# Kernel tuning notes

Hardware: AMD Instinct MI355X
Metric: run time of the kernel (lower is better)

## Reference

```python
import jax, jax.numpy as jnp
import numpy as np

R = 5            # num_relations
NEG_SLOPE = 0.2
N1 = 30000       # layer0 target count
N2 = 15000       # layer1 target count


def brgcn_conv(x_src, x_tgt, edge_index, edge_type, Wj, Wi, att_j, att_i,
               Wq, Wk, Wv, sw, sb, Wrel, heads, outc):
    """One BRGCNConv layer: per-relation GAT edge softmax + bilevel relation attention."""
    N = x_tgt.shape[0]
    hc = heads * outc
    hj = (x_src @ Wj).reshape(-1, heads, outc)   # [Ns,H,C]
    hi = (x_tgt @ Wi).reshape(-1, heads, outc)   # [N,H,C]
    src, tgt = edge_index[0], edge_index[1]
    xj = hj[src]                                  # [E,H,C]
    xi = hi[tgt]                                  # [E,H,C]
    # relation-specific attention logits per edge
    aj = jnp.sum(att_j[edge_type] * xj, axis=-1)  # [E,H]
    ai = jnp.sum(att_i[edge_type] * xi, axis=-1)  # [E,H]
    alpha = jax.nn.leaky_relu(aj + ai, NEG_SLOPE)
    # edge softmax grouped by (target node, relation) == per-relation propagate
    seg = tgt * R + edge_type                     # [E]
    nseg = N * R
    amax = jax.ops.segment_max(alpha, seg, num_segments=nseg)
    amax = jnp.where(jnp.isfinite(amax), amax, 0.0)
    ex = jnp.exp(alpha - amax[seg])
    den = jax.ops.segment_sum(ex, seg, num_segments=nseg)
    w = ex / jnp.maximum(den[seg], 1e-16)         # [E,H]
    msg = (w[:, :, None] * xj).reshape(-1, hc)    # [E,H*C]
    z = jax.ops.segment_sum(msg, seg, num_segments=nseg)
    z = z.reshape(N, R, hc).transpose(1, 0, 2)    # [R,N,H*C]; zero rows where no edges
    # per-relation Q/K/V
    q = jnp.einsum('rnd,rde->rne', z, Wq).reshape(R, N, heads, outc)
    k = jnp.einsum('rnd,rde->rne', z, Wk).reshape(R, N, heads, outc)
    v = jnp.einsum('rnd,rde->rne', z, Wv).reshape(R, N, heads, outc)
    # bilevel relation attention: psi[r,s,n,h] = <q_r, k_s>
    psi = jnp.einsum('rnhc,snhc->rsnh', q, k)
    mask = (psi == 0) & (jnp.sum(psi, axis=1, keepdims=True) != 0)
    prob = jax.nn.softmax(jnp.where(mask, -jnp.inf, psi), axis=1)
    delta = jnp.einsum('rsnh,snhc->rnhc', prob, v).reshape(R, N, hc)
    out = jnp.einsum('rnd,r->nd', delta, Wrel[:, 0])
    # single node type -> node_self[0] applied to every target node
    return out + x_tgt @ sw + sb


def setup_inputs() -> dict:
    key = jax.random.key(0)
    ks = jax.random.split(key, 32)
    H0, C0, H1, C1 = 4, 64, 1, 40
    IN, HC0 = 128, H0 * C0
    NG, N0 = 200000, 100000
    E0, E1 = 300000, 150000
    f = lambda k, s: jax.random.normal(k, s, dtype=jnp.float32) * 0.05
    return dict(
        n_id=jax.random.randint(ks[1], (N0,), 0, NG),
        local_node_idx=jax.random.randint(ks[2], (NG,), 0, NG),
        node_type=jnp.zeros((NG,), dtype=jnp.int32),
        edge_index0=jax.random.randint(ks[3], (2, E0), 0, N1),
        edge_type0=jax.random.randint(ks[4], (E0,), 0, R),
        edge_index1=jax.random.randint(ks[5], (2, E1), 0, N2),
        edge_type1=jax.random.randint(ks[6], (E1,), 0, R),
        emb=f(ks[0], (NG, IN)),
        Wj0=f(ks[7], (IN, HC0)), Wi0=f(ks[8], (IN, HC0)),
        att_j0=f(ks[9], (R, H0, C0)), att_i0=f(ks[10], (R, H0, C0)),
        Wq0=f(ks[11], (R, HC0, HC0)), Wk0=f(ks[12], (R, HC0, HC0)), Wv0=f(ks[13], (R, HC0, HC0)),
        sw0=f(ks[14], (IN, HC0)), sb0=f(ks[15], (HC0,)), Wrel0=f(ks[16], (R, 1)),
        Wj1=f(ks[17], (HC0, C1)), Wi1=f(ks[18], (HC0, C1)),
        att_j1=f(ks[19], (R, H1, C1)), att_i1=f(ks[20], (R, H1, C1)),
        Wq1=f(ks[21], (R, C1, C1)), Wk1=f(ks[22], (R, C1, C1)), Wv1=f(ks[23], (R, C1, C1)),
        sw1=f(ks[24], (HC0, C1)), sb1=f(ks[25], (C1,)), Wrel1=f(ks[26], (R, 1)),
    )


def reference(n_id, local_node_idx, node_type, edge_index0, edge_type0,
              edge_index1, edge_type1, emb,
              Wj0, Wi0, att_j0, att_i0, Wq0, Wk0, Wv0, sw0, sb0, Wrel0,
              Wj1, Wi1, att_j1, att_i1, Wq1, Wk1, Wv1, sw1, sb1, Wrel1):
    # group_input: single node type, all features from the embedding table
    x = emb[local_node_idx[n_id]]
    x1 = brgcn_conv(x, x[:N1], edge_index0, edge_type0, Wj0, Wi0, att_j0, att_i0,
                    Wq0, Wk0, Wv0, sw0, sb0, Wrel0, heads=4, outc=64)
    x1 = jax.nn.relu(x1)  # dropout p=0 in eval
    x2 = brgcn_conv(x1, x1[:N2], edge_index1, edge_type1, Wj1, Wi1, att_j1, att_i1,
                    Wq1, Wk1, Wv1, sw1, sb1, Wrel1, heads=1, outc=40)
    return jax.nn.log_softmax(x2, axis=-1)
```

## Files before the change

### kernel.cpp

```cpp
#include <hip/hip_runtime.h>
#include <hip/hip_bf16.h>

#define DI __device__ __forceinline__

DI float b2f(unsigned short u) {
    union { unsigned int i; float f; } x; x.i = ((unsigned int)u) << 16; return x.f;
}
DI unsigned short f2b(float f) {
    union { float f; unsigned int i; } x; x.f = f;
    unsigned int r = x.i + 0x7fff + ((x.i >> 16) & 1);
    return (unsigned short)(r >> 16);
}
DI float ldin(const void* p, long i, int f32) {
    return f32 ? ((const float*)p)[i] : b2f(((const unsigned short*)p)[i]);
}
DI void stval(float* p, float v) { *p = v; }
DI void stval(unsigned short* p, float v) { *p = f2b(v); }

static constexpr int N1 = 30000, N2 = 15000, R = 5;
static constexpr int IN = 128, HC0 = 256, C1 = 40;
static constexpr float NEGBIG = -1e30f;
static constexpr int LDK = 64;

typedef short bf16x8 __attribute__((ext_vector_type(8)));
typedef float f32x4 __attribute__((ext_vector_type(4)));

__global__ void detect_k(const void* emb, int* flag)
{
    int lane = threadIdx.x;
    int bad = 0;
    for (int j = 0; j < 4; ++j) {
        float f = b2f(((const unsigned short*)emb)[lane * 4 + j]);
        if (!(fabsf(f) < 1e8f)) bad = 1;
    }
    unsigned long long anybad = __ballot(bad != 0);
    if (lane == 0) *flag = (anybad != 0ull) ? 1 : 0;
}

struct PrepJobs {
    const void* src[12];
    unsigned short* dst[12];
    int K[12];
    int N[12];
    int per[12];
};
__global__ __launch_bounds__(256) void prep_all_k(
    PrepJobs J,
    const void* aj0, const void* ai0, const void* aj1, const void* ai1,
    unsigned short* A0j, unsigned short* A0i, unsigned short* A1j, unsigned short* A1i,
    int* __restrict__ cnt, int cntn,
    const int* __restrict__ dflag)
{
    const int f32 = *dflag;
    const int y = blockIdx.y;
    long t = (long)blockIdx.x * 256 + threadIdx.x;
    if (y < 12) {
        if (t >= J.per[y]) return;
        const int K = J.K[y], N = J.N[y];
        long kn = (long)K * N;
        long b = t / kn, rem = t % kn;
        long k = rem / N, n = rem % N;
        J.dst[y][(b * N + n) * K + k] = f2b(ldin(J.src[y], t, f32));
    } else {
        if (t < 20 * 256) {
            int j = (int)(t >> 8), k = (int)(t & 255);
            int h = j & 3, r = j >> 2;
            bool on = (k >> 6) == h;
            A0j[t] = f2b(on ? ldin(aj0, r * 256 + k, f32) : 0.f);
            A0i[t] = f2b(on ? ldin(ai0, r * 256 + k, f32) : 0.f);
        }
        if (t < 5 * 40) {
            A1j[t] = f2b(ldin(aj1, t, f32));
            A1i[t] = f2b(ldin(ai1, t, f32));
        }
        if (t < cntn) cnt[t] = 0;
    }
}

__global__ __launch_bounds__(256) void gather_k(
    const int* __restrict__ n_id, const int* __restrict__ lidx,
    const void* __restrict__ emb, unsigned short* __restrict__ x, int rows,
    const int* __restrict__ dflag)
{
    const int f32 = *dflag;
    long t = (long)blockIdx.x * 256 + threadIdx.x;
    long n = t >> 7, d = t & 127;
    if (n >= rows) return;
    long row = lidx[n_id[n]];
    x[n * IN + d] = f2b(ldin(emb, row * IN + d, f32));
}


DI void stage_fast(const unsigned short* __restrict__ G, int K,
                   unsigned short* S, int wave, int lane)
{
    const int p = lane >> 3;
    const int scol = ((lane & 7) ^ p) * 8;
#pragma unroll
    for (int t = 0; t < 4; ++t) {
        int row = t * 32 + wave * 8 + p;
        const unsigned short* src = G + (long)row * K + scol;
        unsigned short* dst = S + (t * 32 + wave * 8) * LDK;
        __builtin_amdgcn_global_load_lds(
            (const __attribute__((address_space(1))) unsigned int*)src,
            (__attribute__((address_space(3))) unsigned int*)dst, 16, 0, 0);
    }
}
DI void stage_slow(const unsigned short* __restrict__ G, int rows, int K,
                   int r0, int k0, unsigned short* S, int tid)
{
    const int sr = tid >> 1, sq = (tid & 1) * 32;
    const int sx = sr & 7;
    unsigned short* drow = S + sr * LDK;
    const unsigned short* g = G + (long)(r0 + sr) * K + k0 + sq;
    const bool rowok = (r0 + sr) < rows;
    const int s0 = sq >> 3;
    if (rowok && (k0 + sq + 32) <= K) {
        const uint4* gv = (const uint4*)g;
        uint4 a = gv[0], b = gv[1], c = gv[2], d = gv[3];
        *(uint4*)(drow + (((s0 + 0) ^ sx) << 3)) = a;
        *(uint4*)(drow + (((s0 + 1) ^ sx) << 3)) = b;
        *(uint4*)(drow + (((s0 + 2) ^ sx) << 3)) = c;
        *(uint4*)(drow + (((s0 + 3) ^ sx) << 3)) = d;
    } else if (!rowok) {
        uint4 zz = {0u, 0u, 0u, 0u};
        *(uint4*)(drow + (((s0 + 0) ^ sx) << 3)) = zz;
        *(uint4*)(drow + (((s0 + 1) ^ sx) << 3)) = zz;
        *(uint4*)(drow + (((s0 + 2) ^ sx) << 3)) = zz;
        *(uint4*)(drow + (((s0 + 3) ^ sx) << 3)) = zz;
    } else {
#pragma unroll 8
        for (int j = 0; j < 32; ++j) {
            int col = sq + j;
            int k = k0 + col;
            int widx = (((col >> 3) ^ sx) << 3) | (col & 7);
            drow[widx] = (k < K) ? g[j] : (unsigned short)0;
        }
    }
}

DI void stageA(const unsigned short* __restrict__ G, int K,
               unsigned short* S, int wave, int lane)
{
    if (K == 256) {
        const int lrow = lane >> 5, slin = lane & 31;
#pragma unroll
        for (int t = 0; t < 16; ++t) {
            int rbase = wave * 32 + t * 2;
            int row = rbase + lrow;
            const unsigned short* src = G + (long)row * 256 + ((slin ^ (row & 7)) << 3);
            unsigned short* dst = S + rbase * 256;
            __builtin_amdgcn_global_load_lds(
                (const __attribute__((address_space(1))) unsigned int*)src,
                (__attribute__((address_space(3))) unsigned int*)dst, 16, 0, 0);
        }
    } else {
        const int lrow = lane >> 4, slin = lane & 15;
#pragma unroll
        for (int t = 0; t < 8; ++t) {
            int rbase = wave * 32 + t * 4;
            int row = rbase + lrow;
            const unsigned short* src = G + (long)row * 128 + ((slin ^ (row & 7)) << 3);
            unsigned short* dst = S + rbase * 128;
            __builtin_amdgcn_global_load_lds(
                (const __attribute__((address_space(1))) unsigned int*)src,
                (__attribute__((address_space(3))) unsigned int*)dst, 16, 0, 0);
        }
    }
}

__global__ __launch_bounds__(256) void gemm_ares_k(
    const unsigned short* __restrict__ Ab,
    const unsigned short* B0, const unsigned short* B1, const unsigned short* B2,
    unsigned short* C0, unsigned short* C1, unsigned short* C2,
    const void* bias0, const void* bias1, const void* bias2,
    const int* __restrict__ dflag,
    int M, int K, long sA, long sB, long sC)
{
    __shared__ unsigned short As[128 * 256];
    __shared__ unsigned short Bs[128 * LDK];
    const int f32 = *dflag;
    const int tid = threadIdx.x;
    const int lane = tid & 63, wave = tid >> 6;
    const int b = blockIdx.z;
    const int n0 = blockIdx.x * 128, m0 = blockIdx.y * 128;
    const int wm = (wave & 1) * 64, wn = (wave >> 1) * 64;
    const int row16 = lane & 15, quad = lane >> 4;

    stageA(Ab + (long)b * sA + (long)m0 * K, K, As, wave, lane);

#pragma unroll 1
    for (int sel = 0; sel < 3; ++sel) {
        const unsigned short* Bt = (sel == 0 ? B0 : sel == 1 ? B1 : B2)
                                   + (long)b * sB + (long)n0 * K;
        unsigned short* C = (sel == 0 ? C0 : sel == 1 ? C1 : C2) + (long)b * sC;
        const void* bias = sel == 0 ? bias0 : sel == 1 ? bias1 : bias2;
        f32x4 acc[4][4];
#pragma unroll
        for (int i = 0; i < 4; ++i)
#pragma unroll
            for (int j = 0; j < 4; ++j) acc[i][j] = {0.f, 0.f, 0.f, 0.f};

        for (int k0 = 0; k0 < K; k0 += 64) {
            stage_fast(Bt + k0, K, Bs, wave, lane);
            __syncthreads();
#pragma unroll
            for (int ks = 0; ks < 64; ks += 32) {
                const int saw = ((((k0 + ks) >> 3) + quad) ^ (row16 & 7)) << 3;
                const int sbw = (((quad + (ks >> 3)) ^ (row16 & 7)) << 3);
                bf16x8 af[4], bfr[4];
#pragma unroll
                for (int i = 0; i < 4; ++i)
                    af[i] = *(const bf16x8*)(As + (wm + i * 16 + row16) * K + saw);
#pragma unroll
                for (int j = 0; j < 4; ++j)
                    bfr[j] = *(const bf16x8*)(Bs + (wn + j * 16 + row16) * LDK + sbw);
#pragma unroll
                for (int i = 0; i < 4; ++i)
#pragma unroll
                    for (int j = 0; j < 4; ++j)
                        acc[i][j] = __builtin_amdgcn_mfma_f32_16x16x32_bf16(
                            af[i], bfr[j], acc[i][j], 0, 0, 0);
            }
            __syncthreads();
        }
#pragma unroll
        for (int i = 0; i < 4; ++i) {
#pragma unroll
            for (int reg = 0; reg < 4; ++reg) {
                const int gr = m0 + wm + i * 16 + quad * 4 + reg;
                if (gr >= M) continue;
#pragma unroll
                for (int j = 0; j < 4; ++j) {
                    const int gc = n0 + wn + j * 16 + row16;
                    float v = acc[i][j][reg];
                    if (bias) v += ldin(bias, gc, f32);
                    C[(long)gr * 256 + gc] = f2b(v);
                }
            }
        }
    }
}

template <typename OT>
DI void gemm_mfma_body(
    const unsigned short* __restrict__ A, const unsigned short* __restrict__ Bt,
    OT* __restrict__ C, const void* __restrict__ bias, int f32,
    int M, int N, int K, unsigned short* As, unsigned short* Bs)
{
    const int tid = threadIdx.x;
    const int m0 = blockIdx.y * 128, n0 = blockIdx.x * 128;
    const int lane = tid & 63, wave = tid >> 6;
    const int wm = (wave & 1) * 64, wn = (wave >> 1) * 64;
    const int row16 = lane & 15, quad = lane >> 4;
    const bool kfull = (K & 63) == 0;
    const bool fastA = kfull && (m0 + 128 <= M);
    const bool fastB = kfull && (n0 + 128 <= N);
    f32x4 acc[4][4];
#pragma unroll
    for (int i = 0; i < 4; ++i)
#pragma unroll
        for (int j = 0; j < 4; ++j) acc[i][j] = {0.f, 0.f, 0.f, 0.f};

    for (int k0 = 0; k0 < K; k0 += 64) {
        if (fastA) stage_fast(A + (long)m0 * K + k0, K, As, wave, lane);
        else       stage_slow(A, M, K, m0, k0, As, tid);
        if (fastB) stage_fast(Bt + (long)n0 * K + k0, K, Bs, wave, lane);
        else       stage_slow(Bt, N, K, n0, k0, Bs, tid);
        __syncthreads();
#pragma unroll
        for (int ks = 0; ks < 64; ks += 32) {
            const int sw = (((quad + (ks >> 3)) ^ (row16 & 7)) << 3);
            bf16x8 af[4], bfr[4];
#pragma unroll
            for (int i = 0; i < 4; ++i)
                af[i] = *(const bf16x8*)(As + (wm + i * 16 + row16) * LDK + sw);
#pragma unroll
            for (int j = 0; j < 4; ++j)
                bfr[j] = *(const bf16x8*)(Bs + (wn + j * 16 + row16) * LDK + sw);
#pragma unroll
            for (int i = 0; i < 4; ++i)
#pragma unroll
                for (int j = 0; j < 4; ++j)
                    acc[i][j] = __builtin_amdgcn_mfma_f32_16x16x32_bf16(
                        af[i], bfr[j], acc[i][j], 0, 0, 0);
        }
        __syncthreads();
    }
#pragma unroll
    for (int i = 0; i < 4; ++i) {
#pragma unroll
        for (int reg = 0; reg < 4; ++reg) {
            const int gr = m0 + wm + i * 16 + quad * 4 + reg;
            if (gr >= M) continue;
#pragma unroll
            for (int j = 0; j < 4; ++j) {
                const int gc = n0 + wn + j * 16 + row16;
                if (gc >= N) continue;
                float v = acc[i][j][reg];
                if (bias) v += ldin(bias, gc, f32);
                stval(&C[(long)gr * N + gc], v);
            }
        }
    }
}

template <typename OT>
__global__ __launch_bounds__(256) void gemm_mfma3_k(
    const unsigned short* A0, const unsigned short* A1, const unsigned short* A2,
    const unsigned short* Bt0, const unsigned short* Bt1, const unsigned short* Bt2,
    OT* C0, OT* C1, OT* C2,
    const void* bias0, const void* bias1, const void* bias2,
    const int* __restrict__ dflag,
    int M, int N, int K, long sA, long sB, long sC, int nbatch)
{
    __shared__ unsigned short As[128 * LDK];
    __shared__ unsigned short Bs[128 * LDK];
    const int f32 = *dflag;
    const int sel = blockIdx.z / nbatch, b = blockIdx.z % nbatch;
    const unsigned short* A  = (sel == 0 ? A0 : sel == 1 ? A1 : A2) + (long)b * sA;
    const unsigned short* Bt = (sel == 0 ? Bt0 : sel == 1 ? Bt1 : Bt2) + (long)b * sB;
    OT* C = (sel == 0 ? C0 : sel == 1 ? C1 : C2) + (long)b * sC;
    const void* bias = sel == 0 ? bias0 : sel == 1 ? bias1 : bias2;
    gemm_mfma_body<OT>(A, Bt, C, bias, f32, M, N, K, As, Bs);
}

__global__ __launch_bounds__(256) void hist_k(const int* __restrict__ ei, int E, int* __restrict__ cnt)
{
    int e = blockIdx.x * 256 + threadIdx.x;
    if (e < E) atomicAdd(&cnt[ei[E + e]], 1);
}
__global__ __launch_bounds__(256) void scan1_k(
    const int* __restrict__ cnt, int* __restrict__ off, int* __restrict__ bsum, int n)
{
    __shared__ int buf[256];
    int i = blockIdx.x * 256 + threadIdx.x;
    int v = (i < n) ? cnt[i] : 0;
    buf[threadIdx.x] = v;
    __syncthreads();
#pragma unroll
    for (int s = 1; s < 256; s <<= 1) {
        int t = (threadIdx.x >= s) ? buf[threadIdx.x - s] : 0;
        __syncthreads();
        buf[threadIdx.x] += t;
        __syncthreads();
    }
    if (i < n) off[i] = buf[threadIdx.x] - v;
    if (threadIdx.x == 255) bsum[blockIdx.x] = buf[255];
}
__global__ void scan2_k(int* __restrict__ bsum, int nb, int* __restrict__ total_dst)
{
    __shared__ int buf[256];
    int v = (threadIdx.x < nb) ? bsum[threadIdx.x] : 0;
    buf[threadIdx.x] = v;
    __syncthreads();
#pragma unroll
    for (int s = 1; s < 256; s <<= 1) {
        int t = (threadIdx.x >= s) ? buf[threadIdx.x - s] : 0;
        __syncthreads();
        buf[threadIdx.x] += t;
        __syncthreads();
    }
    if (threadIdx.x < nb) bsum[threadIdx.x] = buf[threadIdx.x] - v;
    if (threadIdx.x == 255) *total_dst = buf[255];
}
__global__ __launch_bounds__(256) void scan3_k(
    int* __restrict__ off, int* __restrict__ cursor, const int* __restrict__ bsum,
    int* __restrict__ cnt, int n)
{
    int i = blockIdx.x * 256 + threadIdx.x;
    if (i < n) {
        int v = off[i] + bsum[blockIdx.x];
        off[i] = v;
        cursor[i] = v;
        cnt[i] = 0;
    }
}

__global__ __launch_bounds__(256) void scatter0_k(
    const int* __restrict__ ei, const int* __restrict__ et, int E,
    int* __restrict__ cursor,
    const float* __restrict__ ajn, const float* __restrict__ ain,
    int* __restrict__ src_s, int* __restrict__ rt_s, float* __restrict__ w4_s)
{
    int e = blockIdx.x * 256 + threadIdx.x;
    if (e >= E) return;
    int src = ei[e], tgt = ei[E + e], r = et[e];
    int p = atomicAdd(&cursor[tgt], 1);
    src_s[p] = src; rt_s[p] = r;
    float4 a = *(const float4*)(ajn + (long)src * 20 + r * 4);
    float4 b = *(const float4*)(ain + (long)tgt * 20 + r * 4);
    float4 w;
    float s0 = a.x + b.x, s1 = a.y + b.y, s2 = a.z + b.z, s3 = a.w + b.w;
    s0 = s0 > 0.f ? s0 : 0.2f * s0;  s1 = s1 > 0.f ? s1 : 0.2f * s1;
    s2 = s2 > 0.f ? s2 : 0.2f * s2;  s3 = s3 > 0.f ? s3 : 0.2f * s3;
    w.x = expf(fminf(s0, 60.f)); w.y = expf(fminf(s1, 60.f));
    w.z = expf(fminf(s2, 60.f)); w.w = expf(fminf(s3, 60.f));
    *(float4*)(w4_s + (long)p * 4) = w;
}
__global__ __launch_bounds__(256) void scatter1_k(
    const int* __restrict__ ei, const int* __restrict__ et, int E,
    int* __restrict__ cursor,
    const float* __restrict__ ajn, const float* __restrict__ ain,
    int* __restrict__ src_s, int* __restrict__ rt_s, float* __restrict__ w_s)
{
    int e = blockIdx.x * 256 + threadIdx.x;
    if (e >= E) return;
    int src = ei[e], tgt = ei[E + e], r = et[e];
    int p = atomicAdd(&cursor[tgt], 1);
    src_s[p] = src; rt_s[p] = r;
    float s = ajn[(long)src * 5 + r] + ain[(long)tgt * 5 + r];
    s = s > 0.f ? s : 0.2f * s;
    w_s[p] = expf(fminf(s, 60.f));
}

__global__ __launch_bounds__(256) void aggregate0_k(
    const int* __restrict__ src_s, const int* __restrict__ rt_s,
    const float* __restrict__ w4_s, const int* __restrict__ off,
    const unsigned short* __restrict__ hj,
    unsigned short* __restrict__ z, int Nn)
{
    int tgt = (int)((blockIdx.x * 256u + threadIdx.x) >> 6);
    int lane = threadIdx.x & 63;
    if (tgt >= Nn) return;
    int dd = lane * 4, h = lane >> 4;
    float acc[5][4] = {};
    float den[5] = {};
    int s = off[tgt], epd = off[tgt + 1];
    for (int i = s; i < epd; ++i) {
        int src = src_s[i];
        int r_e = rt_s[i];
        float wgt = w4_s[(long)i * 4 + h];
        ushort4 xj = *(const ushort4*)(hj + (long)src * 256 + dd);
        float x0 = b2f(xj.x), x1 = b2f(xj.y), x2 = b2f(xj.z), x3 = b2f(xj.w);
#pragma unroll
        for (int r = 0; r < 5; ++r) {
            float ws = (r == r_e) ? wgt : 0.f;
            den[r] += ws;
            acc[r][0] += ws * x0; acc[r][1] += ws * x1;
            acc[r][2] += ws * x2; acc[r][3] += ws * x3;
        }
    }
#pragma unroll
    for (int r = 0; r < 5; ++r) {
        float inv = 1.f / fmaxf(den[r], 1e-16f);
        ushort4 o;
        o.x = f2b(acc[r][0] * inv); o.y = f2b(acc[r][1] * inv);
        o.z = f2b(acc[r][2] * inv); o.w = f2b(acc[r][3] * inv);
        *(ushort4*)(z + ((long)r * Nn + tgt) * 256 + dd) = o;
    }
}

__global__ __launch_bounds__(256) void aggregate1_k(
    const int* __restrict__ src_s, const int* __restrict__ rt_s,
    const float* __restrict__ w_s, const int* __restrict__ off,
    const unsigned short* __restrict__ hj,
    unsigned short* __restrict__ z, int Nn)
{
    int tgt = (int)((blockIdx.x * 256u + threadIdx.x) >> 6);
    int lane = threadIdx.x & 63;
    if (tgt >= Nn) return;
    bool act = lane < 40;
    float acc[5] = {};
    float den[5] = {};
    int s = off[tgt], epd = off[tgt + 1];
    for (int i = s; i < epd; ++i) {
        int src = src_s[i];
        int r_e = rt_s[i];
        float wgt = w_s[i];
        float xj = act ? b2f(hj[(long)src * 40 + lane]) : 0.f;
#pragma unroll
        for (int r = 0; r < 5; ++r) {
            float ws = (r == r_e) ? wgt : 0.f;
            den[r] += ws;
            acc[r] += ws * xj;
        }
    }
    if (act) {
#pragma unroll
        for (int r = 0; r < 5; ++r) {
            float inv = 1.f / fmaxf(den[r], 1e-16f);
            z[((long)r * Nn + tgt) * 40 + lane] = f2b(acc[r] * inv);
        }
    }
}

__global__ __launch_bounds__(256) void fused_attn0_k(
    const unsigned short* __restrict__ qb, const unsigned short* __restrict__ kb,
    const unsigned short* __restrict__ vb, const void* __restrict__ wrel,
    unsigned short* __restrict__ x1, int n0, int nloc, int chq,
    const int* __restrict__ dflag)
{
    const int f32 = *dflag;
    int nl = (int)((blockIdx.x * 256u + threadIdx.x) >> 6);
    int lane = threadIdx.x & 63;
    if (nl >= nloc) return;
    int n = n0 + nl;
    int dd = lane * 4;
    float qf[5][4], kf[5][4];
#pragma unroll
    for (int r = 0; r < 5; ++r) {
        ushort4 qv = *(const ushort4*)(qb + ((long)r * chq + nl) * 256 + dd);
        ushort4 kv = *(const ushort4*)(kb + ((long)r * chq + nl) * 256 + dd);
        qf[r][0] = b2f(qv.x); qf[r][1] = b2f(qv.y); qf[r][2] = b2f(qv.z); qf[r][3] = b2f(qv.w);
        kf[r][0] = b2f(kv.x); kf[r][1] = b2f(kv.y); kf[r][2] = b2f(kv.z); kf[r][3] = b2f(kv.w);
    }
    float psi[5][5];
#pragma unroll
    for (int r = 0; r < 5; ++r)
#pragma unroll
        for (int s = 0; s < 5; ++s) {
            float p = qf[r][0] * kf[s][0] + qf[r][1] * kf[s][1] +
                      qf[r][2] * kf[s][2] + qf[r][3] * kf[s][3];
            p += __shfl_xor(p, 1, 64); p += __shfl_xor(p, 2, 64);
            p += __shfl_xor(p, 4, 64); p += __shfl_xor(p, 8, 64);
            psi[r][s] = p;
        }
    float pw[5] = {0.f, 0.f, 0.f, 0.f, 0.f};
#pragma unroll
    for (int r = 0; r < 5; ++r) {
        float rowsum = psi[r][0] + psi[r][1] + psi[r][2] + psi[r][3] + psi[r][4];
        float vals[5], m = NEGBIG;
#pragma unroll
        for (int s = 0; s < 5; ++s) {
            float v = (psi[r][s] == 0.f && rowsum != 0.f) ? NEGBIG : psi[r][s];
            vals[s] = v; m = fmaxf(m, v);
        }
        float es[5], sum = 0.f;
#pragma unroll
        for (int s = 0; s < 5; ++s) { es[s] = expf(vals[s] - m); sum += es[s]; }
        float wr = ldin(wrel, r, f32) / sum;
#pragma unroll
        for (int s = 0; s < 5; ++s) pw[s] += wr * es[s];
    }
    float acc[4] = {0.f, 0.f, 0.f, 0.f};
#pragma unroll
    for (int s = 0; s < 5; ++s) {
        ushort4 vv = *(const ushort4*)(vb + ((long)s * chq + nl) * 256 + dd);
        acc[0] += pw[s] * b2f(vv.x); acc[1] += pw[s] * b2f(vv.y);
        acc[2] += pw[s] * b2f(vv.z); acc[3] += pw[s] * b2f(vv.w);
    }
    ushort4* xp = (ushort4*)(x1 + (long)n * 256 + dd);
    ushort4 sv = *xp;
    sv.x = f2b(fmaxf(b2f(sv.x) + acc[0], 0.f));
    sv.y = f2b(fmaxf(b2f(sv.y) + acc[1], 0.f));
    sv.z = f2b(fmaxf(b2f(sv.z) + acc[2], 0.f));
    sv.w = f2b(fmaxf(b2f(sv.w) + acc[3], 0.f));
    *xp = sv;
}

__global__ __launch_bounds__(256) void fused_attn1_k(
    const unsigned short* __restrict__ qb, const unsigned short* __restrict__ kb,
    const unsigned short* __restrict__ vb, const void* __restrict__ wrel,
    const unsigned short* __restrict__ self1, void* __restrict__ out, int N,
    const int* __restrict__ dflag)
{
    const int f32 = *dflag;
    int n = (int)((blockIdx.x * 256u + threadIdx.x) >> 6);
    int lane = threadIdx.x & 63;
    if (n >= N) return;
    bool act = lane < 40;
    float qf[5], kf[5];
#pragma unroll
    for (int r = 0; r < 5; ++r) {
        long o = ((long)r * N + n) * 40 + lane;
        qf[r] = act ? b2f(qb[o]) : 0.f;
        kf[r] = act ? b2f(kb[o]) : 0.f;
    }
    float psi[5][5];
#pragma unroll
    for (int r = 0; r < 5; ++r)
#pragma unroll
        for (int s = 0; s < 5; ++s) {
            float p = qf[r] * kf[s];
            p += __shfl_xor(p, 1, 64);  p += __shfl_xor(p, 2, 64);
            p += __shfl_xor(p, 4, 64);  p += __shfl_xor(p, 8, 64);
            p += __shfl_xor(p, 16, 64); p += __shfl_xor(p, 32, 64);
            psi[r][s] = p;
        }
    float pw[5] = {0.f, 0.f, 0.f, 0.f, 0.f};
#pragma unroll
    for (int r = 0; r < 5; ++r) {
        float rowsum = psi[r][0] + psi[r][1] + psi[r][2] + psi[r][3] + psi[r][4];
        float vals[5], m = NEGBIG;
#pragma unroll
        for (int s = 0; s < 5; ++s) {
            float v = (psi[r][s] == 0.f && rowsum != 0.f) ? NEGBIG : psi[r][s];
            vals[s] = v; m = fmaxf(m, v);
        }
        float es[5], sum = 0.f;
#pragma unroll
        for (int s = 0; s < 5; ++s) { es[s] = expf(vals[s] - m); sum += es[s]; }
        float wr = ldin(wrel, r, f32) / sum;
#pragma unroll
        for (int s = 0; s < 5; ++s) pw[s] += wr * es[s];
    }
    float val = NEGBIG;
    if (act) {
        float acc = 0.f;
#pragma unroll
        for (int s = 0; s < 5; ++s) acc += pw[s] * b2f(vb[((long)s * N + n) * 40 + lane]);
        val = b2f(self1[(long)n * 40 + lane]) + acc;
    }
    float m = val;
#pragma unroll
    for (int msk = 1; msk < 64; msk <<= 1) m = fmaxf(m, __shfl_xor(m, msk, 64));
    float e = act ? expf(val - m) : 0.f;
#pragma unroll
    for (int msk = 1; msk < 64; msk <<= 1) e += __shfl_xor(e, msk, 64);
    if (act) {
        float r = val - m - logf(e);
        long oidx = (long)n * 40 + lane;
        if (f32) ((float*)out)[oidx] = r;
        else     ((unsigned short*)out)[oidx] = f2b(r);
    }
}

extern "C" void kernel_launch(void* const* d_in, const int* in_sizes, int n_in,
                              void* d_out, int out_size, void* d_ws, size_t ws_size,
                              hipStream_t stream)
{
    const int* n_id = (const int*)d_in[0];
    const int* lidx = (const int*)d_in[1];
    const int* ei0  = (const int*)d_in[3];
    const int* et0  = (const int*)d_in[4];
    const int* ei1  = (const int*)d_in[5];
    const int* et1  = (const int*)d_in[6];
    const void* emb = d_in[7];
    const void* Wj0 = d_in[8];  const void* Wi0 = d_in[9];
    const void* aj0 = d_in[10]; const void* ai0 = d_in[11];
    const void* Wq0 = d_in[12]; const void* Wk0 = d_in[13]; const void* Wv0 = d_in[14];
    const void* sw0 = d_in[15]; const void* sb0 = d_in[16]; const void* Wr0 = d_in[17];
    const void* Wj1 = d_in[18]; const void* Wi1 = d_in[19];
    const void* aj1 = d_in[20]; const void* ai1 = d_in[21];
    const void* Wq1 = d_in[22]; const void* Wk1 = d_in[23]; const void* Wv1 = d_in[24];
    const void* sw1 = d_in[25]; const void* sb1 = d_in[26]; const void* Wr1 = d_in[27];
    const int E0 = in_sizes[4], E1 = in_sizes[6];

    auto al = [](size_t b) { return (b + 255) & ~(size_t)255; };

    const size_t P_total =
        al((size_t)R * N1 * HC0 * 2) +
        al((size_t)N1 * HC0 * 2) +
        2 * al((size_t)N1 * 20 * 4) +
        3 * al((size_t)(N1 + 1) * 4) +
        al(256 * 4) +
        2 * al((size_t)E0 * 4) +
        al((size_t)E0 * 16) +
        3 * al((size_t)HC0 * IN * 2) +
        3 * al((size_t)R * HC0 * HC0 * 2) +
        3 * al((size_t)C1 * HC0 * 2) +
        3 * al((size_t)R * C1 * C1 * 2) +
        2 * al(20 * 256 * 2) + 2 * al(5 * 40 * 2) +
        al(256);

    int CH = 15000;
    {
        size_t need = 3 * al((size_t)R * CH * HC0 * 2) + P_total + (16u << 20);
        if (need > ws_size) CH = 7500;
    }
    const size_t QB = al((size_t)R * CH * HC0 * 2);

    char* w = (char*)d_ws;
    unsigned short* qc = (unsigned short*)(w);
    unsigned short* kc = (unsigned short*)(w + QB);
    unsigned short* vc = (unsigned short*)(w + 2 * QB);
    unsigned short* x30k = (unsigned short*)(w);
    unsigned short* hj0  = (unsigned short*)(w + al((size_t)N1 * IN * 2));
    unsigned short* hi0  = (unsigned short*)((char*)hj0 + al((size_t)N1 * HC0 * 2));
    size_t o1 = 0;
    auto take1 = [&](size_t b) { char* p = w + o1; o1 += (b + 255) & ~(size_t)255; return p; };
    unsigned short* hj1   = (unsigned short*)take1((size_t)N2 * C1 * 2);
    unsigned short* hi1   = (unsigned short*)take1((size_t)N2 * C1 * 2);
    unsigned short* self1 = (unsigned short*)take1((size_t)N2 * C1 * 2);
    float* ajn1 = (float*)take1((size_t)N2 * R * 4);
    float* ain1 = (float*)take1((size_t)N2 * R * 4);
    unsigned short* z1  = (unsigned short*)take1((size_t)R * N2 * C1 * 2);
    unsigned short* q1b = (unsigned short*)take1((size_t)R * N2 * C1 * 2);
    unsigned short* k1b = (unsigned short*)take1((size_t)R * N2 * C1 * 2);
    unsigned short* v1b = (unsigned short*)take1((size_t)R * N2 * C1 * 2);
    size_t o = 3 * QB;
    auto take = [&](size_t b) { char* p = w + o; o += (b + 255) & ~(size_t)255; return p; };
    unsigned short* z0 = (unsigned short*)take((size_t)R * N1 * HC0 * 2);
    unsigned short* x1 = (unsigned short*)take((size_t)N1 * HC0 * 2);
    float* ajn0 = (float*)take((size_t)N1 * 20 * 4);
    float* ain0 = (float*)take((size_t)N1 * 20 * 4);
    int* cnt    = (int*)take((size_t)(N1 + 1) * 4);
    int* off    = (int*)take((size_t)(N1 + 1) * 4);
    int* cursor = (int*)take((size_t)(N1 + 1) * 4);
    int* bsum   = (int*)take(256 * 4);
    int* src_s  = (int*)take((size_t)E0 * 4);
    int* rt_s   = (int*)take((size_t)E0 * 4);
    float* w4_s = (float*)take((size_t)E0 * 16);
    unsigned short* wjt0 = (unsigned short*)take((size_t)HC0 * IN * 2);
    unsigned short* wit0 = (unsigned short*)take((size_t)HC0 * IN * 2);
    unsigned short* swt0 = (unsigned short*)take((size_t)HC0 * IN * 2);
    unsigned short* wqt0 = (unsigned short*)take((size_t)R * HC0 * HC0 * 2);
    unsigned short* wkt0 = (unsigned short*)take((size_t)R * HC0 * HC0 * 2);
    unsigned short* wvt0 = (unsigned short*)take((size_t)R * HC0 * HC0 * 2);
    unsigned short* wjt1 = (unsigned short*)take((size_t)C1 * HC0 * 2);
    unsigned short* wit1 = (unsigned short*)take((size_t)C1 * HC0 * 2);
    unsigned short* swt1 = (unsigned short*)take((size_t)C1 * HC0 * 2);
    unsigned short* wqt1 = (unsigned short*)take((size_t)R * C1 * C1 * 2);
    unsigned short* wkt1 = (unsigned short*)take((size_t)R * C1 * C1 * 2);
    unsigned short* wvt1 = (unsigned short*)take((size_t)R * C1 * C1 * 2);
    unsigned short* atA0j = (unsigned short*)take(20 * 256 * 2);
    unsigned short* atA0i = (unsigned short*)take(20 * 256 * 2);
    unsigned short* atA1j = (unsigned short*)take(5 * 40 * 2);
    unsigned short* atA1i = (unsigned short*)take(5 * 40 * 2);
    int* dflag = (int*)take(256);

    detect_k<<<1, 64, 0, stream>>>(emb, dflag);

    {
        PrepJobs J;
        const void* srcs[12] = {Wj0, Wi0, sw0, Wq0, Wk0, Wv0, Wj1, Wi1, sw1, Wq1, Wk1, Wv1};
        unsigned short* dsts[12] = {wjt0, wit0, swt0, wqt0, wkt0, wvt0,
                                    wjt1, wit1, swt1, wqt1, wkt1, wvt1};
        int Ks[12] = {IN, IN, IN, HC0, HC0, HC0, HC0, HC0, HC0, C1, C1, C1};
        int Ns[12] = {HC0, HC0, HC0, HC0, HC0, HC0, C1, C1, C1, C1, C1, C1};
        int pers[12] = {IN * HC0, IN * HC0, IN * HC0,
                        R * HC0 * HC0, R * HC0 * HC0, R * HC0 * HC0,
                        HC0 * C1, HC0 * C1, HC0 * C1,
                        R * C1 * C1, R * C1 * C1, R * C1 * C1};
        for (int i = 0; i < 12; ++i) {
            J.src[i] = srcs[i]; J.dst[i] = dsts[i];
            J.K[i] = Ks[i]; J.N[i] = Ns[i]; J.per[i] = pers[i];
        }
        int xb = (R * HC0 * HC0 + 255) / 256;
        prep_all_k<<<dim3((unsigned)xb, 13), 256, 0, stream>>>(
            J, aj0, ai0, aj1, ai1, atA0j, atA0i, atA1j, atA1i, cnt, N1 + 1, dflag);
    }

    gather_k<<<(int)(((long)N1 * IN + 255) / 256), 256, 0, stream>>>(n_id, lidx, emb, x30k, N1, dflag);
    gemm_ares_k<<<dim3(2, (N1 + 127) / 128, 1), 256, 0, stream>>>(
        x30k, wjt0, wit0, swt0, hj0, hi0, x1, nullptr, nullptr, sb0,
        dflag, N1, IN, 0, 0, 0);
    gemm_mfma3_k<float><<<dim3(1, (N1 + 127) / 128, 2), 256, 0, stream>>>(
        hj0, hi0, hi0, atA0j, atA0i, atA0i, ajn0, ain0, ain0, nullptr, nullptr, nullptr,
        dflag, N1, 20, HC0, 0, 0, 0, 1);

    hist_k<<<(E0 + 255) / 256, 256, 0, stream>>>(ei0, E0, cnt);
    {
        int nb = (N1 + 255) / 256;
        scan1_k<<<nb, 256, 0, stream>>>(cnt, off, bsum, N1);
        scan2_k<<<1, 256, 0, stream>>>(bsum, nb, off + N1);
        scan3_k<<<nb, 256, 0, stream>>>(off, cursor, bsum, cnt, N1);
    }
    scatter0_k<<<(E0 + 255) / 256, 256, 0, stream>>>(ei0, et0, E0, cursor, ajn0, ain0, src_s, rt_s, w4_s);
    aggregate0_k<<<(N1 + 3) / 4, 256, 0, stream>>>(src_s, rt_s, w4_s, off, hj0, z0, N1);

    {
        const int nch = N1 / CH;
        for (int c = 0; c < nch; ++c) {
            const unsigned short* zc = z0 + (long)c * CH * HC0;
            gemm_ares_k<<<dim3(2, (CH + 127) / 128, R), 256, 0, stream>>>(
                zc, wqt0, wkt0, wvt0, qc, kc, vc, nullptr, nullptr, nullptr,
                dflag, CH, HC0, (long)N1 * HC0, (long)HC0 * HC0, (long)CH * HC0);
            fused_attn0_k<<<(CH + 3) / 4, 256, 0, stream>>>(qc, kc, vc, Wr0, x1, c * CH, CH, CH, dflag);
        }
    }

    gemm_mfma3_k<unsigned short><<<dim3(1, (N2 + 127) / 128, 3), 256, 0, stream>>>(
        x1, x1, x1, wjt1, wit1, swt1, hj1, hi1, self1, nullptr, nullptr, sb1,
        dflag, N2, C1, HC0, 0, 0, 0, 1);
    gemm_mfma3_k<float><<<dim3(1, (N2 + 127) / 128, 2), 256, 0, stream>>>(
        hj1, hi1, hi1, atA1j, atA1i, atA1i, ajn1, ain1, ain1, nullptr, nullptr, nullptr,
        dflag, N2, 5, C1, 0, 0, 0, 1);

    hist_k<<<(E1 + 255) / 256, 256, 0, stream>>>(ei1, E1, cnt);
    {
        int nb = (N2 + 255) / 256;
        scan1_k<<<nb, 256, 0, stream>>>(cnt, off, bsum, N2);
        scan2_k<<<1, 256, 0, stream>>>(bsum, nb, off + N2);
        scan3_k<<<nb, 256, 0, stream>>>(off, cursor, bsum, cnt, N2);
    }
    scatter1_k<<<(E1 + 255) / 256, 256, 0, stream>>>(ei1, et1, E1, cursor, ajn1, ain1, src_s, rt_s, w4_s);
    aggregate1_k<<<(N2 + 3) / 4, 256, 0, stream>>>(src_s, rt_s, w4_s, off, hj1, z1, N2);

    {
        long sA = (long)N2 * C1, sB = (long)C1 * C1, sC = (long)N2 * C1;
        gemm_mfma3_k<unsigned short><<<dim3(1, (N2 + 127) / 128, 3 * R), 256, 0, stream>>>(
            z1, z1, z1, wqt1, wkt1, wvt1, q1b, k1b, v1b, nullptr, nullptr, nullptr,
            dflag, N2, C1, C1, sA, sB, sC, R);
    }
    fused_attn1_k<<<(N2 + 3) / 4, 256, 0, stream>>>(q1b, k1b, v1b, Wr1, self1, d_out, N2, dflag);
}
```

Baseline: 657.3 us.

## Halve GEMM M-tile and read B fragments directly from global memory

Replaces the resident-A GEMM with a templated variant that uses 64-row M tiles (less LDS, more blocks) and drops the B staging through LDS. B fragments now load straight from global/L2 per wave, with no per-K-step barriers. This aims to raise occupancy and remove the synchronisation overhead, at the cost of redundant global reads of the weight tiles across waves and blocks.

```diff
diff --git a/kernel.cpp b/kernel.cpp
--- a/kernel.cpp
+++ b/kernel.cpp
@@ -139,93 +139,90 @@
     }
 }
 
-DI void stageA(const unsigned short* __restrict__ G, int K,
-               unsigned short* S, int wave, int lane)
-{
-    if (K == 256) {
-        const int lrow = lane >> 5, slin = lane & 31;
-#pragma unroll
-        for (int t = 0; t < 16; ++t) {
-            int rbase = wave * 32 + t * 2;
-            int row = rbase + lrow;
-            const unsigned short* src = G + (long)row * 256 + ((slin ^ (row & 7)) << 3);
-            unsigned short* dst = S + rbase * 256;
-            __builtin_amdgcn_global_load_lds(
-                (const __attribute__((address_space(1))) unsigned int*)src,
-                (__attribute__((address_space(3))) unsigned int*)dst, 16, 0, 0);
-        }
-    } else {
-        const int lrow = lane >> 4, slin = lane & 15;
-#pragma unroll
-        for (int t = 0; t < 8; ++t) {
-            int rbase = wave * 32 + t * 4;
-            int row = rbase + lrow;
-            const unsigned short* src = G + (long)row * 128 + ((slin ^ (row & 7)) << 3);
-            unsigned short* dst = S + rbase * 128;
-            __builtin_amdgcn_global_load_lds(
-                (const __attribute__((address_space(1))) unsigned int*)src,
-                (__attribute__((address_space(3))) unsigned int*)dst, 16, 0, 0);
-        }
-    }
-}
-
-__global__ __launch_bounds__(256) void gemm_ares_k(
+template <int KK>
+__global__ __launch_bounds__(256) void gemm_ares2_k(
     const unsigned short* __restrict__ Ab,
     const unsigned short* B0, const unsigned short* B1, const unsigned short* B2,
     unsigned short* C0, unsigned short* C1, unsigned short* C2,
     const void* bias0, const void* bias1, const void* bias2,
     const int* __restrict__ dflag,
-    int M, int K, long sA, long sB, long sC)
-{
-    __shared__ unsigned short As[128 * 256];
-    __shared__ unsigned short Bs[128 * LDK];
+    int M, long sA, long sB, long sC)
+{
+    __shared__ unsigned short As[64 * KK];
     const int f32 = *dflag;
     const int tid = threadIdx.x;
     const int lane = tid & 63, wave = tid >> 6;
     const int b = blockIdx.z;
-    const int n0 = blockIdx.x * 128, m0 = blockIdx.y * 128;
-    const int wm = (wave & 1) * 64, wn = (wave >> 1) * 64;
+    const int n0 = blockIdx.x * 128, m0 = blockIdx.y * 64;
+    const int wm = (wave & 1) * 32, wn = (wave >> 1) * 64;
     const int row16 = lane & 15, quad = lane >> 4;
 
-    stageA(Ab + (long)b * sA + (long)m0 * K, K, As, wave, lane);
+    {
+        const unsigned short* Gb = Ab + (long)b * sA + (long)m0 * KK;
+        if (KK == 256) {
+            const int lrow = lane >> 5, slin = lane & 31;
+#pragma unroll
+            for (int t = 0; t < 8; ++t) {
+                int rbase = wave * 16 + t * 2;
+                int row = rbase + lrow;
+                const unsigned short* src = Gb + (long)row * 256 + ((slin ^ (row & 7)) << 3);
+                unsigned short* dst = As + rbase * 256;
+                __builtin_amdgcn_global_load_lds(
+                    (const __attribute__((address_space(1))) unsigned int*)src,
+                    (__attribute__((address_space(3))) unsigned int*)dst, 16, 0, 0);
+            }
+        } else {
+            const int lrow = lane >> 4, slin = lane & 15;
+#pragma unroll
+            for (int t = 0; t < 4; ++t) {
+                int rbase = wave * 16 + t * 4;
+                int row = rbase + lrow;
+                const unsigned short* src = Gb + (long)row * 128 + ((slin ^ (row & 7)) << 3);
+                unsigned short* dst = As + rbase * 128;
+                __builtin_amdgcn_global_load_lds(
+                    (const __attribute__((address_space(1))) unsigned int*)src,
+                    (__attribute__((address_space(3))) unsigned int*)dst, 16, 0, 0);
+            }
+        }
+    }
+    __syncthreads();
 
 #pragma unroll 1
     for (int sel = 0; sel < 3; ++sel) {
         const unsigned short* Bt = (sel == 0 ? B0 : sel == 1 ? B1 : B2)
-                                   + (long)b * sB + (long)n0 * K;
+                                   + (long)b * sB + (long)n0 * KK;
         unsigned short* C = (sel == 0 ? C0 : sel == 1 ? C1 : C2) + (long)b * sC;
         const void* bias = sel == 0 ? bias0 : sel == 1 ? bias1 : bias2;
-        f32x4 acc[4][4];
-#pragma unroll
-        for (int i = 0; i < 4; ++i)
+        const unsigned short* brow[4];
+#pragma unroll
+        for (int j = 0; j < 4; ++j)
+            brow[j] = Bt + (long)(wn + j * 16 + row16) * KK + quad * 8;
+
+        f32x4 acc[2][4];
+#pragma unroll
+        for (int i = 0; i < 2; ++i)
 #pragma unroll
             for (int j = 0; j < 4; ++j) acc[i][j] = {0.f, 0.f, 0.f, 0.f};
 
-        for (int k0 = 0; k0 < K; k0 += 64) {
-            stage_fast(Bt + k0, K, Bs, wave, lane);
-            __syncthreads();
-#pragma unroll
-            for (int ks = 0; ks < 64; ks += 32) {
-                const int saw = ((((k0 + ks) >> 3) + quad) ^ (row16 & 7)) << 3;
-                const int sbw = (((quad + (ks >> 3)) ^ (row16 & 7)) << 3);
-                bf16x8 af[4], bfr[4];
-#pragma unroll
-                for (int i = 0; i < 4; ++i)
-                    af[i] = *(const bf16x8*)(As + (wm + i * 16 + row16) * K + saw);
+#pragma unroll
+        for (int kk = 0; kk < KK; kk += 32) {
+            const int saw = ((((kk) >> 3) + quad) ^ (row16 & 7)) << 3;
+            bf16x8 af[2], bfr[4];
+#pragma unroll
+            for (int i = 0; i < 2; ++i)
+                af[i] = *(const bf16x8*)(As + (wm + i * 16 + row16) * KK + saw);
+#pragma unroll
+            for (int j = 0; j < 4; ++j)
+                bfr[j] = *(const bf16x8*)(brow[j] + kk);
+#pragma unroll
+            for (int i = 0; i < 2; ++i)
 #pragma unroll
                 for (int j = 0; j < 4; ++j)
-                    bfr[j] = *(const bf16x8*)(Bs + (wn + j * 16 + row16) * LDK + sbw);
-#pragma unroll
-                for (int i = 0; i < 4; ++i)
-#pragma unroll
-                    for (int j = 0; j < 4; ++j)
-                        acc[i][j] = __builtin_amdgcn_mfma_f32_16x16x32_bf16(
-                            af[i], bfr[j], acc[i][j], 0, 0, 0);
-            }
-            __syncthreads();
-        }
-#pragma unroll
-        for (int i = 0; i < 4; ++i) {
+                    acc[i][j] = __builtin_amdgcn_mfma_f32_16x16x32_bf16(
+                        af[i], bfr[j], acc[i][j], 0, 0, 0);
+        }
+#pragma unroll
+        for (int i = 0; i < 2; ++i) {
 #pragma unroll
             for (int reg = 0; reg < 4; ++reg) {
                 const int gr = m0 + wm + i * 16 + quad * 4 + reg;
@@ -733,9 +730,9 @@
     }
 
     gather_k<<<(int)(((long)N1 * IN + 255) / 256), 256, 0, stream>>>(n_id, lidx, emb, x30k, N1, dflag);
-    gemm_ares_k<<<dim3(2, (N1 + 127) / 128, 1), 256, 0, stream>>>(
+    gemm_ares2_k<128><<<dim3(2, (N1 + 63) / 64, 1), 256, 0, stream>>>(
         x30k, wjt0, wit0, swt0, hj0, hi0, x1, nullptr, nullptr, sb0,
-        dflag, N1, IN, 0, 0, 0);
+        dflag, N1, 0, 0, 0);
     gemm_mfma3_k<float><<<dim3(1, (N1 + 127) / 128, 2), 256, 0, stream>>>(
         hj0, hi0, hi0, atA0j, atA0i, atA0i, ajn0, ain0, ain0, nullptr, nullptr, nullptr,
         dflag, N1, 20, HC0, 0, 0, 0, 1);
@@ -754,9 +751,9 @@
         const int nch = N1 / CH;
         for (int c = 0; c < nch; ++c) {
             const unsigned short* zc = z0 + (long)c * CH * HC0;
-            gemm_ares_k<<<dim3(2, (CH + 127) / 128, R), 256, 0, stream>>>(
+            gemm_ares2_k<256><<<dim3(2, (CH + 63) / 64, R), 256, 0, stream>>>(
                 zc, wqt0, wkt0, wvt0, qc, kc, vc, nullptr, nullptr, nullptr,
-                dflag, CH, HC0, (long)N1 * HC0, (long)HC0 * HC0, (long)CH * HC0);
+                dflag, CH, (long)N1 * HC0, (long)HC0 * HC0, (long)CH * HC0);
             fused_attn0_k<<<(CH + 3) / 4, 256, 0, stream>>>(qc, kc, vc, Wr0, x1, c * CH, CH, CH, dflag);
         }
     }
```

Result: slower. 799.4 us (+21.6%).
